# Kernel tuning notes

Measured on AMD Instinct MI355X. Metric: run time of the kernel, lower is better.

The kernel has to match this reference:

```python
import jax, jax.numpy as jnp
import numpy as np

# Config matching init_kwargs
DIM = 768; NH = 12; K = 16; BASE_LR = 1.0  # mini_batch_size K, ttt_base_lr


def _ln(x, g, b, eps=1e-6):
    mu = x.mean(-1, keepdims=True)
    var = x.var(-1, keepdims=True)
    return g * (x - mu) * jax.lax.rsqrt(var + eps) + b


def _ln_l2_bwd(x, tgt, g, b, eps=1e-6):
    # grad wrt x of ||LN(x; g, b) - tgt||^2 (TTT fused layernorm-l2 backward)
    D = x.shape[-1]
    mu = x.mean(-1, keepdims=True)
    var = x.var(-1, keepdims=True)
    std = jnp.sqrt(var + eps)
    xh = (x - mu) / std
    gout = (g * xh + b) - tgt
    gxh = gout * g
    return (D * gxh - gxh.sum(-1, keepdims=True) - xh * (gxh * xh).sum(-1, keepdims=True)) / (D * std)


def _rotary(x, fc):
    # x: [..., N, hd]; fc: [N, hd//2] complex
    xr = x.reshape(*x.shape[:-1], -1, 2)
    xc = jax.lax.complex(xr[..., 0], xr[..., 1]) * fc
    return jnp.stack([jnp.real(xc), jnp.imag(xc)], -1).reshape(x.shape)


def setup_inputs() -> dict:
    key = jax.random.key(0)
    ks = jax.random.split(key, 6)
    B, N, C = 16, 1024, DIM
    nh2, hd, W2 = 2 * NH, C // NH, 2 * C
    f = jnp.float32
    x = jax.random.normal(ks[0], (B, N, C), f)
    qkv_w = jax.random.normal(ks[1], (C, 3 * C), f) * (1.0 / np.sqrt(C))
    proj_w = jax.random.normal(ks[2], (C, C), f) * (1.0 / np.sqrt(C))
    proj_b = jnp.zeros((C,), f)
    W1 = jax.random.normal(ks[3], (nh2, hd, hd), f) * 0.02  # per-head fast-weight init
    b1 = jnp.zeros((nh2, 1, hd), f)
    ttt_ln_w = jnp.ones((nh2, hd), f)
    ttt_ln_b = jnp.zeros((nh2, hd), f)
    post_ln_w = jnp.ones((W2,), f)
    post_ln_b = jnp.zeros((W2,), f)
    lr_w = jax.random.normal(ks[4], (W2, nh2), f) * 0.02  # learnable ttt lr projection
    lr_b = jnp.zeros((nh2,), f)
    token_idx_delta = jnp.zeros((K,), f)  # learnable token-idx offset, init 0
    return dict(x=x, qkv_w=qkv_w, proj_w=proj_w, proj_b=proj_b, W1=W1, b1=b1,
                ttt_ln_w=ttt_ln_w, ttt_ln_b=ttt_ln_b, post_ln_w=post_ln_w, post_ln_b=post_ln_b,
                lr_w=lr_w, lr_b=lr_b, token_idx_delta=token_idx_delta)


def reference(x, qkv_w, proj_w, proj_b, W1, b1, ttt_ln_w, ttt_ln_b,
              post_ln_w, post_ln_b, lr_w, lr_b, token_idx_delta):
    B, N, C = x.shape
    nh2, hd, W2 = 2 * NH, C // NH, 2 * C
    nmb = N // K
    # fused QKV projection (no bias)
    q, k, v = jnp.split(x @ qkv_w, 3, axis=-1)  # each [B,N,C]
    # bidirectional: concat forward stream with token-flipped backward stream
    qq = jnp.concatenate([q, jnp.flip(q, axis=-2)], axis=-1)  # [B,N,2C]
    kk = jnp.concatenate([k, jnp.flip(k, axis=-2)], axis=-1)
    vv = jnp.concatenate([v, jnp.flip(v, axis=-2)], axis=-1)
    xx = jnp.concatenate([x, jnp.flip(x, axis=-2)], axis=-1)

    def heads(t):  # [B,N,2C] -> [B,nh2,N,hd]
        return t.reshape(B, N, nh2, hd).transpose(0, 2, 1, 3)
    XQ, XK, XV = heads(qq), heads(kk), heads(vv)

    # rotary embedding with position_ids % mini_batch_size
    pos = (jnp.arange(N) % K).astype(jnp.float32)
    inv = 1.0 / (10000.0 ** (jnp.arange(0, hd, 2, dtype=jnp.float32) / hd))
    ang = pos[:, None] * inv[None, :]
    fc = jax.lax.complex(jnp.cos(ang), jnp.sin(ang))  # [N, hd//2]
    XQ = _rotary(XQ, fc)
    XK = _rotary(XK, fc)

    def mb(t):  # [B,nh2,N,hd] -> [B,nh2,nmb,K,hd]
        return t.reshape(B, nh2, nmb, K, hd)
    XQ, XK, XV = mb(XQ), mb(XK), mb(XV)

    # eta: token_idx (1/i, learnable offset, clipped) x per-token learnable lr
    Xr = xx.reshape(B, nmb, K, W2)
    lr = jax.nn.sigmoid(Xr @ lr_w + lr_b) * (BASE_LR / hd)  # [B,nmb,K,nh2]
    tok = jnp.clip(1.0 / jnp.arange(1, K + 1, dtype=jnp.float32) + token_idx_delta, 0.0)
    # eta[b,h,m,i,j] = tok[i] * lr[b,m,j,h]
    eta = tok[None, None, None, :, None] * lr.transpose(0, 3, 1, 2)[:, :, :, None, :]  # [B,nh2,nmb,K,K]

    mask = jnp.tril(jnp.ones((K, K), x.dtype))  # AR mask within mini-batch
    g = ttt_ln_w[None, :, None, :]   # [1,nh2,1,hd]
    bt = ttt_ln_b[None, :, None, :]
    W1_0 = jnp.broadcast_to(W1[None], (B, nh2, hd, hd))
    b1_0 = jnp.broadcast_to(b1[None], (B, nh2, 1, hd))

    def step(carry, inp):
        W, bb = carry
        xq, xk, xv, et = inp  # [B,nh2,K,hd] x3, [B,nh2,K,K]
        Z1 = xk @ W + bb
        grad = _ln_l2_bwd(Z1, xv - xk, g, bt)  # dl/dZ1
        attn = jnp.einsum('bhid,bhjd->bhij', xq, xk) * mask
        b1_bar = bb - (et * mask) @ grad
        Z1_bar = xq @ W - (et * attn) @ grad + b1_bar
        last = et[..., -1, :, None]  # eta row of last token [B,nh2,K,1]
        Wn = W - jnp.einsum('bhkd,bhke->bhde', last * xk, grad)
        bn = bb - (last * grad).sum(-2, keepdims=True)
        out = xq + _ln(Z1_bar, g, bt)  # residual + per-head TTT layernorm
        return (Wn, bn), out

    xs = (XQ.transpose(2, 0, 1, 3, 4), XK.transpose(2, 0, 1, 3, 4),
          XV.transpose(2, 0, 1, 3, 4), eta.transpose(2, 0, 1, 3, 4))
    _, Z = jax.lax.scan(step, (W1_0, b1_0), xs)  # Z: [nmb,B,nh2,K,hd]

    Z = Z.transpose(1, 2, 0, 3, 4).reshape(B, nh2, N, hd).transpose(0, 2, 1, 3).reshape(B, N, W2)
    Z = _ln(Z, post_ln_w, post_ln_b)  # mult_norm post-norm
    zf, zb = jnp.split(Z, 2, axis=-1)
    out = zf * jnp.flip(zb, axis=-2)  # merge forward / flipped-backward streams
    return out @ proj_w + proj_b
```

## Files before the change

### kernel.cpp

```cpp
#include <hip/hip_runtime.h>
#include <hip/hip_bf16.h>

#define Bq   16
#define Nseq 1024
#define Cdim 768
#define NH2  24
#define W2D  1536
#define KB   16
#define NMB  64

typedef short bfrag8 __attribute__((ext_vector_type(8)));
typedef short bfrag4 __attribute__((ext_vector_type(4)));
typedef float f32x4  __attribute__((ext_vector_type(4)));

__device__ __forceinline__ short f2bs(float x) {
  union { __hip_bfloat16 b; short s; } u;
  u.b = __float2bfloat16(x);
  return u.s;
}
__device__ __forceinline__ bfrag8 cvt8(const float* v) {
  bfrag8 r;
#pragma unroll
  for (int i = 0; i < 8; ++i) r[i] = f2bs(v[i]);
  return r;
}
__device__ __forceinline__ bfrag4 cvt4(float a, float b, float c, float d) {
  bfrag4 r;
  r[0] = f2bs(a); r[1] = f2bs(b); r[2] = f2bs(c); r[3] = f2bs(d);
  return r;
}
__device__ __forceinline__ void async_copy16(const void* g, void* l) {
  __builtin_amdgcn_global_load_lds((const __attribute__((address_space(1))) void*)g,
                                   (__attribute__((address_space(3))) void*)l, 16, 0, 0);
}

#if defined(__has_builtin)
#  if __has_builtin(__builtin_amdgcn_mfma_f32_16x16x16bf16_1k)
#    define HAVE_MFMA16X16X16 1
#  endif
#endif
__device__ __forceinline__ f32x4 mfma16(bfrag4 a, bfrag4 b, f32x4 c) {
#ifdef HAVE_MFMA16X16X16
  return __builtin_amdgcn_mfma_f32_16x16x16bf16_1k(a, b, c, 0, 0, 0);
#else
  f32x4 d;
  asm volatile("v_mfma_f32_16x16x16_bf16 %0, %1, %2, %3"
               : "=v"(d) : "v"(a), "v"(b), "v"(c));
  return d;
#endif
}

__device__ __forceinline__ void lds_fence() {
  asm volatile("s_waitcnt lgkmcnt(0)" ::: "memory");
  __builtin_amdgcn_sched_barrier(0);
}

template<int N>
__device__ __forceinline__ float dpp_ror(float x) {
  union { float f; int i; } a, r;
  a.f = x;
  r.i = __builtin_amdgcn_update_dpp(0, a.i, 0x120 | N, 0xF, 0xF, 1);
  return r.f;
}
__device__ __forceinline__ float rowsum16(float x) {
  x += dpp_ror<8>(x);
  x += dpp_ror<4>(x);
  x += dpp_ror<2>(x);
  x += dpp_ror<1>(x);
  return x;
}

__global__ __launch_bounds__(256) void gemm_bf16_kernel(
    const __hip_bfloat16* __restrict__ A,
    const __hip_bfloat16* __restrict__ Bt,
    const float* __restrict__ bias, float* __restrict__ C,
    int M, int Kd, int Nd)
{
  __shared__ short sA[128 * 64];
  __shared__ short sB[128 * 64];
  const int t = threadIdx.x;
  const int w = t >> 6, lane = t & 63;
  const int quad = lane >> 4, li = lane & 15;
  const int wm = w & 1, wn = w >> 1;
  const int m0 = blockIdx.y * 128, n0 = blockIdx.x * 128;

  f32x4 acc[4][4];
#pragma unroll
  for (int mt = 0; mt < 4; ++mt)
#pragma unroll
    for (int nt = 0; nt < 4; ++nt) acc[mt][nt] = (f32x4){0.f, 0.f, 0.f, 0.f};

  const __hip_bfloat16* Ab = A + (size_t)m0 * Kd;
  const __hip_bfloat16* Bb = Bt + (size_t)n0 * Kd;

#pragma unroll 1
  for (int k0 = 0; k0 < Kd; k0 += 64) {
    __syncthreads();
#pragma unroll
    for (int i = 0; i < 4; ++i) {
      int c = i * 256 + t;
      int row = c >> 3;
      int gl = (c & 7) ^ (row & 7);
      async_copy16(Ab + (size_t)row * Kd + k0 + gl * 8, &sA[c * 8]);
      async_copy16(Bb + (size_t)row * Kd + k0 + gl * 8, &sB[c * 8]);
    }
    __syncthreads();
#pragma unroll
    for (int ks = 0; ks < 2; ++ks) {
      bfrag8 aF[4], bF[4];
#pragma unroll
      for (int mt = 0; mt < 4; ++mt) {
        int row = wm * 64 + mt * 16 + li;
        int gi = (ks * 4 + quad) ^ (row & 7);
        aF[mt] = *(const bfrag8*)(&sA[row * 64 + gi * 8]);
      }
#pragma unroll
      for (int nt = 0; nt < 4; ++nt) {
        int row = wn * 64 + nt * 16 + li;
        int gi = (ks * 4 + quad) ^ (row & 7);
        bF[nt] = *(const bfrag8*)(&sB[row * 64 + gi * 8]);
      }
#pragma unroll
      for (int mt = 0; mt < 4; ++mt)
#pragma unroll
        for (int nt = 0; nt < 4; ++nt)
          acc[mt][nt] = __builtin_amdgcn_mfma_f32_16x16x32_bf16(aF[mt], bF[nt], acc[mt][nt], 0, 0, 0);
    }
  }

#pragma unroll
  for (int mt = 0; mt < 4; ++mt)
#pragma unroll
    for (int nt = 0; nt < 4; ++nt) {
      int ncol = n0 + wn * 64 + nt * 16 + li;
      float bv = bias ? bias[ncol] : 0.f;
#pragma unroll
      for (int r = 0; r < 4; ++r) {
        int mrow = m0 + wm * 64 + mt * 16 + quad * 4 + r;
        C[(size_t)mrow * Nd + ncol] = acc[mt][nt][r] + bv;
      }
    }
}

__global__ __launch_bounds__(256) void cast_bf16_kernel(
    const float* __restrict__ in, __hip_bfloat16* __restrict__ out, int n4)
{
  int i = blockIdx.x * 256 + threadIdx.x;
  if (i >= n4) return;
  float4 v = ((const float4*)in)[i];
  union { short b[4]; short4 s; } u;
  u.b[0] = f2bs(v.x); u.b[1] = f2bs(v.y); u.b[2] = f2bs(v.z); u.b[3] = f2bs(v.w);
  ((short4*)out)[i] = u.s;
}

__global__ __launch_bounds__(256) void transpose_cast_kernel(
    const float* __restrict__ B, __hip_bfloat16* __restrict__ Bt, int Kd, int Nd)
{
  __shared__ float tl[64][65];
  int k0 = blockIdx.x * 64, n0 = blockIdx.y * 64;
  int tx = threadIdx.x & 63, ty = threadIdx.x >> 6;
#pragma unroll
  for (int i = 0; i < 16; ++i) {
    int k = ty + i * 4;
    tl[k][tx] = B[(size_t)(k0 + k) * Nd + n0 + tx];
  }
  __syncthreads();
#pragma unroll
  for (int i = 0; i < 16; ++i) {
    int n = ty + i * 4;
    Bt[(size_t)(n0 + n) * Kd + k0 + tx] = __float2bfloat16(tl[tx][n]);
  }
}

__global__ __launch_bounds__(64) void lr_kernel(
    const float* __restrict__ x, const float* __restrict__ lr_w,
    const float* __restrict__ lr_b, float* __restrict__ lrout)
{
  const int row = blockIdx.x;
  const int b = row >> 10, n = row & 1023;
  const int l = threadIdx.x;
  const float* x1 = x + (size_t)row * Cdim;
  const float* x2 = x + (size_t)(b * Nseq + (Nseq - 1 - n)) * Cdim;

  float acc[NH2];
#pragma unroll
  for (int hh = 0; hh < NH2; ++hh) acc[hh] = 0.f;

#pragma unroll 1
  for (int i = 0; i < 12; ++i) {
    int c = l + 64 * i;
    float xv1 = x1[c];
    float xv2 = x2[c];
    const float4* w1 = (const float4*)(lr_w + (size_t)c * NH2);
    const float4* w2 = (const float4*)(lr_w + (size_t)(Cdim + c) * NH2);
#pragma unroll
    for (int q4 = 0; q4 < 6; ++q4) {
      float4 wa = w1[q4], wb = w2[q4];
      acc[q4 * 4 + 0] += xv1 * wa.x + xv2 * wb.x;
      acc[q4 * 4 + 1] += xv1 * wa.y + xv2 * wb.y;
      acc[q4 * 4 + 2] += xv1 * wa.z + xv2 * wb.z;
      acc[q4 * 4 + 3] += xv1 * wa.w + xv2 * wb.w;
    }
  }
#pragma unroll
  for (int hh = 0; hh < NH2; ++hh) {
    float s = rowsum16(acc[hh]);
    s += __shfl_xor(s, 16);
    s += __shfl_xor(s, 32);
    acc[hh] = s;
  }
  float mine = 0.f;
#pragma unroll
  for (int hh = 0; hh < NH2; ++hh) mine = (l == hh) ? acc[hh] : mine;
  if (l < NH2) {
    float a = mine + lr_b[l];
    float sg = 1.f / (1.f + expf(-a));
    lrout[(size_t)row * NH2 + l] = sg * (1.f / 64.f);
  }
}

__global__ __launch_bounds__(64, 1) void ttt_scan_kernel(
    const float* __restrict__ qkv,
    const float* __restrict__ lrg,
    const float* __restrict__ W1,
    const float* __restrict__ b1g,
    const float* __restrict__ lnw,
    const float* __restrict__ lnb,
    const float* __restrict__ tid,
    float* __restrict__ Zout)
{
  __shared__ float sQ[16 * 68], sK[16 * 68], sV[16 * 68];

  const int l = threadIdx.x;
  const int quad = l >> 4, li = l & 15;
  const int bh = blockIdx.x, b = bh / NH2, h = bh % NH2;
  const int chan = (h < 12) ? h * 64 : (h - 12) * 64;
  const bool flip = (h >= 12);
  const int bN = b * Nseq;

  float Wf[4][4][4];
  bfrag4 wB[4][4];
#pragma unroll
  for (int t = 0; t < 4; ++t)
#pragma unroll
    for (int kk = 0; kk < 4; ++kk) {
#pragma unroll
      for (int j = 0; j < 4; ++j)
        Wf[t][kk][j] = W1[h * 4096 + (kk * 16 + quad * 4 + j) * 64 + t * 16 + li];
      wB[t][kk] = cvt4(Wf[t][kk][0], Wf[t][kk][1], Wf[t][kk][2], Wf[t][kk][3]);
    }
  float bC[4], gv[4], bt_[4];
#pragma unroll
  for (int t = 0; t < 4; ++t) {
    bC[t]  = b1g[h * 64 + t * 16 + li];
    gv[t]  = lnw[h * 64 + t * 16 + li];
    bt_[t] = lnb[h * 64 + t * 16 + li];
  }

  float tokL;
  {
    float tk = 1.f / (float)(li + 1) + tid[li];
    tokL = tk > 0.f ? tk : 0.f;
  }
  float t15 = 1.f / 16.f + tid[15];
  t15 = t15 > 0.f ? t15 : 0.f;

  float c8[8], s8[8];
  {
    int pos = l >> 2;
#pragma unroll
    for (int pl = 0; pl < 8; ++pl) {
      int p = (l & 3) * 8 + pl;
      float inv = __expf(-((float)(2 * p) * (1.f / 64.f)) * 9.210340371976184f);
      float a = (float)pos * inv;
      c8[pl] = cosf(a);
      s8[pl] = sinf(a);
    }
  }

  float4 pf[3][4];
  float pflr[4];
  {
    int nn = l >> 2;
    int grow = flip ? (bN + Nseq - 1 - nn) : (bN + nn);
#pragma unroll
    for (int a = 0; a < 3; ++a) {
      const float* bse = qkv + (size_t)grow * 2304 + chan + a * 768 + (l & 3) * 16;
#pragma unroll
      for (int i = 0; i < 4; ++i) pf[a][i] = ((const float4*)bse)[i];
    }
#pragma unroll
    for (int r = 0; r < 4; ++r)
      pflr[r] = lrg[(size_t)(bN + quad * 4 + r) * NH2 + h];
  }

#pragma unroll 1
  for (int m = 0; m < NMB; ++m) {
    const int n0 = m * KB;

#pragma unroll
    for (int a = 0; a < 3; ++a) {
      float v16[16];
      *(float4*)(v16)      = pf[a][0]; *(float4*)(v16 + 4)  = pf[a][1];
      *(float4*)(v16 + 8)  = pf[a][2]; *(float4*)(v16 + 12) = pf[a][3];
      if (a < 2) {
#pragma unroll
        for (int pl = 0; pl < 8; ++pl) {
          float e = v16[2 * pl], o = v16[2 * pl + 1];
          v16[2 * pl]     = e * c8[pl] - o * s8[pl];
          v16[2 * pl + 1] = o * c8[pl] + e * s8[pl];
        }
      }
      float* dst = (a == 0 ? sQ : (a == 1 ? sK : sV)) + (l >> 2) * 68 + (l & 3) * 16;
#pragma unroll
      for (int i = 0; i < 4; ++i) ((f32x4*)dst)[i] = *(f32x4*)(v16 + 4 * i);
    }
    float lr4[4];
#pragma unroll
    for (int r = 0; r < 4; ++r) lr4[r] = pflr[r];
    lds_fence();

    if (m < NMB - 1) {
      int nn = (m + 1) * KB + (l >> 2);
      int grow = flip ? (bN + Nseq - 1 - nn) : (bN + nn);
#pragma unroll
      for (int a = 0; a < 3; ++a) {
        const float* bse = qkv + (size_t)grow * 2304 + chan + a * 768 + (l & 3) * 16;
#pragma unroll
        for (int i = 0; i < 4; ++i) pf[a][i] = ((const float4*)bse)[i];
      }
#pragma unroll
      for (int r = 0; r < 4; ++r)
        pflr[r] = lrg[(size_t)(bN + (m + 1) * KB + quad * 4 + r) * NH2 + h];
    }

    bfrag4 aQ4[4], aK4[4];
#pragma unroll
    for (int kk = 0; kk < 4; ++kk) {
      f32x4 q4 = *(const f32x4*)(&sQ[li * 68 + kk * 16 + quad * 4]);
      f32x4 k4 = *(const f32x4*)(&sK[li * 68 + kk * 16 + quad * 4]);
      aQ4[kk] = cvt4(q4[0], q4[1], q4[2], q4[3]);
      aK4[kk] = cvt4(k4[0], k4[1], k4[2], k4[3]);
    }
    float kC[4][4], vC[4][4];
#pragma unroll
    for (int t = 0; t < 4; ++t)
#pragma unroll
      for (int r = 0; r < 4; ++r) {
        int off = (quad * 4 + r) * 68 + t * 16 + li;
        kC[t][r] = sK[off]; vC[t][r] = sV[off];
      }

    f32x4 accZ[4], accQ[4];
#pragma unroll
    for (int t = 0; t < 4; ++t) {
      accZ[t] = (f32x4){0.f, 0.f, 0.f, 0.f};
      accQ[t] = (f32x4){0.f, 0.f, 0.f, 0.f};
#pragma unroll
      for (int kk = 0; kk < 4; ++kk) {
        accZ[t] = mfma16(aK4[kk], wB[t][kk], accZ[t]);
        accQ[t] = mfma16(aQ4[kk], wB[t][kk], accQ[t]);
      }
    }
    f32x4 accAT = (f32x4){0.f, 0.f, 0.f, 0.f};
#pragma unroll
    for (int kk = 0; kk < 4; ++kk)
      accAT = mfma16(aK4[kk], aQ4[kk], accAT);

    bfrag4 aCoef;
    {
      float cf[4];
#pragma unroll
      for (int r = 0; r < 4; ++r) {
        int j = quad * 4 + r;
        cf[r] = (j <= li) ? (-tokL * (accAT[r] + 1.f)) : 0.f;
      }
      aCoef = cvt4(cf[0], cf[1], cf[2], cf[3]);
    }

    float gs[4][4];
#pragma unroll
    for (int r = 0; r < 4; ++r) {
      float zt[4], xht[4], gxht[4];
      float s1 = 0.f, s2 = 0.f;
#pragma unroll
      for (int t = 0; t < 4; ++t) {
        zt[t] = accZ[t][r] + bC[t];
        s1 += zt[t];
        s2 += zt[t] * zt[t];
      }
      s1 = rowsum16(s1);
      s2 = rowsum16(s2);
      float mu = s1 * 0.015625f;
      float var = s2 * 0.015625f - mu * mu;
      float rstd = rsqrtf(var + 1e-6f);
      float r1 = 0.f, r2 = 0.f;
#pragma unroll
      for (int t = 0; t < 4; ++t) {
        xht[t] = (zt[t] - mu) * rstd;
        float gout = gv[t] * xht[t] + bt_[t] - (vC[t][r] - kC[t][r]);
        gxht[t] = gout * gv[t];
        r1 += gxht[t];
        r2 += gxht[t] * xht[t];
      }
      r1 = rowsum16(r1);
      r2 = rowsum16(r2);
      float lrr = lr4[r];
#pragma unroll
      for (int t = 0; t < 4; ++t) {
        float gd = (64.f * gxht[t] - r1 - xht[t] * r2) * rstd * 0.015625f;
        gs[t][r] = lrr * gd;
      }
    }

    bfrag4 bGrad[4], aXk[4];
#pragma unroll
    for (int t = 0; t < 4; ++t) {
      bGrad[t] = cvt4(gs[t][0], gs[t][1], gs[t][2], gs[t][3]);
      aXk[t]   = cvt4(kC[t][0], kC[t][1], kC[t][2], kC[t][3]);
    }

    f32x4 zb[4];
#pragma unroll
    for (int t = 0; t < 4; ++t) {
      f32x4 acc = accQ[t];
#pragma unroll
      for (int r = 0; r < 4; ++r) acc[r] += bC[t];
      zb[t] = mfma16(aCoef, bGrad[t], acc);
    }
#pragma unroll
    for (int r = 0; r < 4; ++r) {
      float s1 = 0.f, s2 = 0.f;
#pragma unroll
      for (int t = 0; t < 4; ++t) { s1 += zb[t][r]; s2 += zb[t][r] * zb[t][r]; }
      s1 = rowsum16(s1);
      s2 = rowsum16(s2);
      float mu = s1 * 0.015625f;
      float var = s2 * 0.015625f - mu * mu;
      float rstd = rsqrtf(var + 1e-6f);
#pragma unroll
      for (int t = 0; t < 4; ++t) {
        float qv = sQ[(quad * 4 + r) * 68 + t * 16 + li];
        float outv = qv + gv[t] * (zb[t][r] - mu) * rstd + bt_[t];
        Zout[(size_t)(bN + n0 + quad * 4 + r) * W2D + h * 64 + t * 16 + li] = outv;
      }
    }

#pragma unroll
    for (int mt = 0; mt < 4; ++mt)
#pragma unroll
      for (int t = 0; t < 4; ++t) {
        f32x4 g = mfma16(aXk[mt], bGrad[t], (f32x4){0.f, 0.f, 0.f, 0.f});
#pragma unroll
        for (int r = 0; r < 4; ++r) Wf[t][mt][r] -= t15 * g[r];
        wB[t][mt] = cvt4(Wf[t][mt][0], Wf[t][mt][1], Wf[t][mt][2], Wf[t][mt][3]);
      }
#pragma unroll
    for (int t = 0; t < 4; ++t) {
      float g0 = gs[t][0] + gs[t][1] + gs[t][2] + gs[t][3];
      g0 += __shfl_xor(g0, 16);
      g0 += __shfl_xor(g0, 32);
      bC[t] -= t15 * g0;
    }
  }
}

__global__ __launch_bounds__(256) void postln_mult_kernel(
    const float* __restrict__ Z, const float* __restrict__ wv,
    const float* __restrict__ bb, __hip_bfloat16* __restrict__ hbuf)
{
  __shared__ float red[16];
  const int pair = blockIdx.x;
  const int b = pair >> 9, n = pair & 511;
  const size_t r1 = (size_t)b * Nseq + n;
  const size_t r2 = (size_t)b * Nseq + (Nseq - 1 - n);
  const float* z1 = Z + r1 * W2D;
  const float* z2 = Z + r2 * W2D;
  const int t = threadIdx.x;

  float v1[6], v2[6];
  float s1a = 0.f, s2a = 0.f, s1b = 0.f, s2b = 0.f;
#pragma unroll
  for (int r = 0; r < 6; ++r) {
    int c = t + 256 * r;
    float a = z1[c]; v1[r] = a; s1a += a; s2a += a * a;
    float d = z2[c]; v2[r] = d; s1b += d; s2b += d * d;
  }
#pragma unroll
  for (int o = 1; o < 64; o <<= 1) {
    s1a += __shfl_xor(s1a, o); s2a += __shfl_xor(s2a, o);
    s1b += __shfl_xor(s1b, o); s2b += __shfl_xor(s2b, o);
  }
  if ((t & 63) == 0) {
    int w = t >> 6;
    red[w] = s1a; red[4 + w] = s2a; red[8 + w] = s1b; red[12 + w] = s2b;
  }
  __syncthreads();
  s1a = red[0] + red[1] + red[2] + red[3];
  s2a = red[4] + red[5] + red[6] + red[7];
  s1b = red[8] + red[9] + red[10] + red[11];
  s2b = red[12] + red[13] + red[14] + red[15];
  float mu1 = s1a * (1.f / 1536.f);
  float var1 = s2a * (1.f / 1536.f) - mu1 * mu1;
  float rstd1 = rsqrtf(var1 + 1e-6f);
  float mu2 = s1b * (1.f / 1536.f);
  float var2 = s2b * (1.f / 1536.f) - mu2 * mu2;
  float rstd2 = rsqrtf(var2 + 1e-6f);
#pragma unroll
  for (int r = 0; r < 3; ++r) {
    int c = t + 256 * r;
    float a1  = wv[c] * (v1[r] - mu1) * rstd1 + bb[c];
    float a1b = wv[c + 768] * (v1[r + 3] - mu1) * rstd1 + bb[c + 768];
    float a2  = wv[c] * (v2[r] - mu2) * rstd2 + bb[c];
    float a2b = wv[c + 768] * (v2[r + 3] - mu2) * rstd2 + bb[c + 768];
    union { __hip_bfloat16 h; short s; } u1, u2;
    u1.h = __float2bfloat16(a1 * a2b);
    u2.h = __float2bfloat16(a2 * a1b);
    ((short*)hbuf)[r1 * Cdim + c] = u1.s;
    ((short*)hbuf)[r2 * Cdim + c] = u2.s;
  }
}

extern "C" void kernel_launch(void* const* d_in, const int* in_sizes, int n_in,
                              void* d_out, int out_size, void* d_ws, size_t ws_size,
                              hipStream_t stream)
{
  const float* x         = (const float*)d_in[0];
  const float* qkv_w     = (const float*)d_in[1];
  const float* proj_w    = (const float*)d_in[2];
  const float* proj_b    = (const float*)d_in[3];
  const float* W1        = (const float*)d_in[4];
  const float* b1        = (const float*)d_in[5];
  const float* ttt_ln_w  = (const float*)d_in[6];
  const float* ttt_ln_b  = (const float*)d_in[7];
  const float* post_ln_w = (const float*)d_in[8];
  const float* post_ln_b = (const float*)d_in[9];
  const float* lr_w      = (const float*)d_in[10];
  const float* lr_b      = (const float*)d_in[11];
  const float* tid       = (const float*)d_in[12];
  float* out = (float*)d_out;
  float* ws  = (float*)d_ws;

  float* qkv   = ws;
  float* lrbuf = ws + 37748736;
  float* Zbuf  = ws + 38141952;
  __hip_bfloat16* xbf    = (__hip_bfloat16*)(ws + 38141952);
  __hip_bfloat16* wqkv_t = (__hip_bfloat16*)(ws + 44433408);
  __hip_bfloat16* hbf    = (__hip_bfloat16*)(ws + 25165824);
  __hip_bfloat16* wproj_t= (__hip_bfloat16*)(ws + 37748736);

  const int Mrows = Bq * Nseq;

  cast_bf16_kernel<<<(Mrows * Cdim / 4 + 255) / 256, 256, 0, stream>>>(x, xbf, Mrows * Cdim / 4);
  {
    dim3 g(Cdim / 64, 3 * Cdim / 64);
    transpose_cast_kernel<<<g, 256, 0, stream>>>(qkv_w, wqkv_t, Cdim, 3 * Cdim);
  }
  {
    dim3 g(3 * Cdim / 128, Mrows / 128);
    gemm_bf16_kernel<<<g, 256, 0, stream>>>(xbf, wqkv_t, nullptr, qkv, Mrows, Cdim, 3 * Cdim);
  }
  lr_kernel<<<Mrows, 64, 0, stream>>>(x, lr_w, lr_b, lrbuf);

  ttt_scan_kernel<<<Bq * NH2, 64, 0, stream>>>(qkv, lrbuf, W1, b1, ttt_ln_w, ttt_ln_b, tid, Zbuf);

  postln_mult_kernel<<<Bq * Nseq / 2, 256, 0, stream>>>(Zbuf, post_ln_w, post_ln_b, hbf);
  {
    dim3 g(Cdim / 64, Cdim / 64);
    transpose_cast_kernel<<<g, 256, 0, stream>>>(proj_w, wproj_t, Cdim, Cdim);
  }
  {
    dim3 g(Cdim / 128, Mrows / 128);
    gemm_bf16_kernel<<<g, 256, 0, stream>>>(hbf, wproj_t, proj_b, out, Mrows, Cdim, Cdim);
  }
}
```

Before: 616.7 us.

## Double-buffer TTT scan LDS staging with transposed copies and remap GEMM blocks per XCD

The TTT scan kernel now double-buffers its Q/K/V LDS tiles and prefetches two mini-batches ahead, so the next chunk is staged while the current one is computed. It also stores transposed copies of Q, K and V so the per-column operand reads become vectorized f32x4 loads instead of scalar strided reads. The bias update is moved earlier. Separately, the GEMM launch becomes a 1D grid whose block index is remapped round-robin across the 8 XCDs for better L2 locality. The cost is more LDS, extra transposed LDS writes, and higher register pressure in a single-wave kernel.

```diff
diff --git a/kernel.cpp b/kernel.cpp
--- a/kernel.cpp
+++ b/kernel.cpp
@@ -74,7 +74,7 @@
     const __hip_bfloat16* __restrict__ A,
     const __hip_bfloat16* __restrict__ Bt,
     const float* __restrict__ bias, float* __restrict__ C,
-    int M, int Kd, int Nd)
+    int M, int Kd, int Nd, int gx)
 {
   __shared__ short sA[128 * 64];
   __shared__ short sB[128 * 64];
@@ -82,7 +82,11 @@
   const int w = t >> 6, lane = t & 63;
   const int quad = lane >> 4, li = lane & 15;
   const int wm = w & 1, wn = w >> 1;
-  const int m0 = blockIdx.y * 128, n0 = blockIdx.x * 128;
+
+  const int nwg = gridDim.x;
+  const int q8 = nwg >> 3;
+  const int lid = ((int)blockIdx.x & 7) * q8 + ((int)blockIdx.x >> 3);
+  const int m0 = (lid / gx) * 128, n0 = (lid % gx) * 128;
 
   f32x4 acc[4][4];
 #pragma unroll
@@ -229,7 +233,11 @@
     const float* __restrict__ tid,
     float* __restrict__ Zout)
 {
-  __shared__ float sQ[16 * 68], sK[16 * 68], sV[16 * 68];
+  __shared__ float sQb[2][16 * 68];
+  __shared__ float sKb[2][16 * 68];
+  __shared__ float sQT[2][64 * 20];
+  __shared__ float sKT[2][64 * 20];
+  __shared__ float sVT[2][64 * 20];
 
   const int l = threadIdx.x;
   const int quad = l >> 4, li = l & 15;
@@ -237,6 +245,7 @@
   const int chan = (h < 12) ? h * 64 : (h - 12) * 64;
   const bool flip = (h >= 12);
   const int bN = b * Nseq;
+  const int stok = l >> 2, sc0 = (l & 3) * 16;
 
   float Wf[4][4][4];
   bfrag4 wB[4][4];
@@ -267,37 +276,30 @@
 
   float c8[8], s8[8];
   {
-    int pos = l >> 2;
 #pragma unroll
     for (int pl = 0; pl < 8; ++pl) {
       int p = (l & 3) * 8 + pl;
       float inv = __expf(-((float)(2 * p) * (1.f / 64.f)) * 9.210340371976184f);
-      float a = (float)pos * inv;
+      float a = (float)stok * inv;
       c8[pl] = cosf(a);
       s8[pl] = sinf(a);
     }
   }
 
   float4 pf[3][4];
-  float pflr[4];
-  {
-    int nn = l >> 2;
+  float lrcur[4], pfl[4];
+
+  auto issue_qkv = [&](int mt) {
+    int nn = mt * KB + stok;
     int grow = flip ? (bN + Nseq - 1 - nn) : (bN + nn);
 #pragma unroll
     for (int a = 0; a < 3; ++a) {
-      const float* bse = qkv + (size_t)grow * 2304 + chan + a * 768 + (l & 3) * 16;
+      const float* bse = qkv + (size_t)grow * 2304 + chan + a * 768 + sc0;
 #pragma unroll
       for (int i = 0; i < 4; ++i) pf[a][i] = ((const float4*)bse)[i];
     }
-#pragma unroll
-    for (int r = 0; r < 4; ++r)
-      pflr[r] = lrg[(size_t)(bN + quad * 4 + r) * NH2 + h];
-  }
-
-#pragma unroll 1
-  for (int m = 0; m < NMB; ++m) {
-    const int n0 = m * KB;
-
+  };
+  auto stage = [&](int buf) {
 #pragma unroll
     for (int a = 0; a < 3; ++a) {
       float v16[16];
@@ -311,45 +313,73 @@
           v16[2 * pl + 1] = o * c8[pl] + e * s8[pl];
         }
       }
-      float* dst = (a == 0 ? sQ : (a == 1 ? sK : sV)) + (l >> 2) * 68 + (l & 3) * 16;
-#pragma unroll
-      for (int i = 0; i < 4; ++i) ((f32x4*)dst)[i] = *(f32x4*)(v16 + 4 * i);
+      if (a == 0) {
+        float* dst = &sQb[buf][stok * 68 + sc0];
+#pragma unroll
+        for (int i = 0; i < 4; ++i) ((f32x4*)dst)[i] = *(f32x4*)(v16 + 4 * i);
+#pragma unroll
+        for (int i = 0; i < 16; ++i) sQT[buf][(sc0 + i) * 20 + stok] = v16[i];
+      } else if (a == 1) {
+        float* dst = &sKb[buf][stok * 68 + sc0];
+#pragma unroll
+        for (int i = 0; i < 4; ++i) ((f32x4*)dst)[i] = *(f32x4*)(v16 + 4 * i);
+#pragma unroll
+        for (int i = 0; i < 16; ++i) sKT[buf][(sc0 + i) * 20 + stok] = v16[i];
+      } else {
+#pragma unroll
+        for (int i = 0; i < 16; ++i) sVT[buf][(sc0 + i) * 20 + stok] = v16[i];
+      }
+    }
+  };
+
+  issue_qkv(0);
+#pragma unroll
+  for (int r = 0; r < 4; ++r) lrcur[r] = lrg[(size_t)(bN + quad * 4 + r) * NH2 + h];
+  stage(0);
+  issue_qkv(1);
+#pragma unroll
+  for (int r = 0; r < 4; ++r) pfl[r] = lrg[(size_t)(bN + KB + quad * 4 + r) * NH2 + h];
+  lds_fence();
+
+#pragma unroll 1
+  for (int m = 0; m < NMB; ++m) {
+    const int n0 = m * KB;
+    const int cur = m & 1, alt = cur ^ 1;
+
+    f32x4 q4[4], k4[4];
+#pragma unroll
+    for (int kk = 0; kk < 4; ++kk) {
+      k4[kk] = *(const f32x4*)(&sKb[cur][li * 68 + kk * 16 + quad * 4]);
+      q4[kk] = *(const f32x4*)(&sQb[cur][li * 68 + kk * 16 + quad * 4]);
+    }
+    f32x4 kC[4], vC[4];
+#pragma unroll
+    for (int t = 0; t < 4; ++t) {
+      kC[t] = *(const f32x4*)(&sKT[cur][(t * 16 + li) * 20 + quad * 4]);
+      vC[t] = *(const f32x4*)(&sVT[cur][(t * 16 + li) * 20 + quad * 4]);
     }
     float lr4[4];
 #pragma unroll
-    for (int r = 0; r < 4; ++r) lr4[r] = pflr[r];
-    lds_fence();
+    for (int r = 0; r < 4; ++r) lr4[r] = lrcur[r];
 
     if (m < NMB - 1) {
-      int nn = (m + 1) * KB + (l >> 2);
-      int grow = flip ? (bN + Nseq - 1 - nn) : (bN + nn);
-#pragma unroll
-      for (int a = 0; a < 3; ++a) {
-        const float* bse = qkv + (size_t)grow * 2304 + chan + a * 768 + (l & 3) * 16;
-#pragma unroll
-        for (int i = 0; i < 4; ++i) pf[a][i] = ((const float4*)bse)[i];
-      }
-#pragma unroll
-      for (int r = 0; r < 4; ++r)
-        pflr[r] = lrg[(size_t)(bN + (m + 1) * KB + quad * 4 + r) * NH2 + h];
+      stage(alt);
+#pragma unroll
+      for (int r = 0; r < 4; ++r) lrcur[r] = pfl[r];
+      if (m < NMB - 2) {
+        issue_qkv(m + 2);
+#pragma unroll
+        for (int r = 0; r < 4; ++r)
+          pfl[r] = lrg[(size_t)(bN + (m + 2) * KB + quad * 4 + r) * NH2 + h];
+      }
     }
 
     bfrag4 aQ4[4], aK4[4];
 #pragma unroll
     for (int kk = 0; kk < 4; ++kk) {
-      f32x4 q4 = *(const f32x4*)(&sQ[li * 68 + kk * 16 + quad * 4]);
-      f32x4 k4 = *(const f32x4*)(&sK[li * 68 + kk * 16 + quad * 4]);
-      aQ4[kk] = cvt4(q4[0], q4[1], q4[2], q4[3]);
-      aK4[kk] = cvt4(k4[0], k4[1], k4[2], k4[3]);
-    }
-    float kC[4][4], vC[4][4];
-#pragma unroll
-    for (int t = 0; t < 4; ++t)
-#pragma unroll
-      for (int r = 0; r < 4; ++r) {
-        int off = (quad * 4 + r) * 68 + t * 16 + li;
-        kC[t][r] = sK[off]; vC[t][r] = sV[off];
-      }
+      aK4[kk] = cvt4(k4[kk][0], k4[kk][1], k4[kk][2], k4[kk][3]);
+      aQ4[kk] = cvt4(q4[kk][0], q4[kk][1], q4[kk][2], q4[kk][3]);
+    }
 
     f32x4 accZ[4], accQ[4];
 #pragma unroll
@@ -428,6 +458,19 @@
       for (int r = 0; r < 4; ++r) acc[r] += bC[t];
       zb[t] = mfma16(aCoef, bGrad[t], acc);
     }
+
+#pragma unroll
+    for (int t = 0; t < 4; ++t) {
+      float g0 = gs[t][0] + gs[t][1] + gs[t][2] + gs[t][3];
+      g0 += __shfl_xor(g0, 16);
+      g0 += __shfl_xor(g0, 32);
+      bC[t] -= t15 * g0;
+    }
+
+    f32x4 qC[4];
+#pragma unroll
+    for (int t = 0; t < 4; ++t)
+      qC[t] = *(const f32x4*)(&sQT[cur][(t * 16 + li) * 20 + quad * 4]);
 #pragma unroll
     for (int r = 0; r < 4; ++r) {
       float s1 = 0.f, s2 = 0.f;
@@ -440,8 +483,7 @@
       float rstd = rsqrtf(var + 1e-6f);
 #pragma unroll
       for (int t = 0; t < 4; ++t) {
-        float qv = sQ[(quad * 4 + r) * 68 + t * 16 + li];
-        float outv = qv + gv[t] * (zb[t][r] - mu) * rstd + bt_[t];
+        float outv = qC[t][r] + gv[t] * (zb[t][r] - mu) * rstd + bt_[t];
         Zout[(size_t)(bN + n0 + quad * 4 + r) * W2D + h * 64 + t * 16 + li] = outv;
       }
     }
@@ -455,13 +497,8 @@
         for (int r = 0; r < 4; ++r) Wf[t][mt][r] -= t15 * g[r];
         wB[t][mt] = cvt4(Wf[t][mt][0], Wf[t][mt][1], Wf[t][mt][2], Wf[t][mt][3]);
       }
-#pragma unroll
-    for (int t = 0; t < 4; ++t) {
-      float g0 = gs[t][0] + gs[t][1] + gs[t][2] + gs[t][3];
-      g0 += __shfl_xor(g0, 16);
-      g0 += __shfl_xor(g0, 32);
-      bC[t] -= t15 * g0;
-    }
+
+    lds_fence();
   }
 }
 
@@ -557,8 +594,9 @@
     transpose_cast_kernel<<<g, 256, 0, stream>>>(qkv_w, wqkv_t, Cdim, 3 * Cdim);
   }
   {
-    dim3 g(3 * Cdim / 128, Mrows / 128);
-    gemm_bf16_kernel<<<g, 256, 0, stream>>>(xbf, wqkv_t, nullptr, qkv, Mrows, Cdim, 3 * Cdim);
+    int gx = 3 * Cdim / 128;
+    int nwg = gx * (Mrows / 128);
+    gemm_bf16_kernel<<<nwg, 256, 0, stream>>>(xbf, wqkv_t, nullptr, qkv, Mrows, Cdim, 3 * Cdim, gx);
   }
   lr_kernel<<<Mrows, 64, 0, stream>>>(x, lr_w, lr_b, lrbuf);
 
@@ -570,7 +608,8 @@
     transpose_cast_kernel<<<g, 256, 0, stream>>>(proj_w, wproj_t, Cdim, Cdim);
   }
   {
-    dim3 g(Cdim / 128, Mrows / 128);
-    gemm_bf16_kernel<<<g, 256, 0, stream>>>(hbf, wproj_t, proj_b, out, Mrows, Cdim, Cdim);
-  }
-}
+    int gx = Cdim / 128;
+    int nwg = gx * (Mrows / 128);
+    gemm_bf16_kernel<<<nwg, 256, 0, stream>>>(hbf, wproj_t, proj_b, out, Mrows, Cdim, Cdim, gx);
+  }
+}
```

Result: slower. 653.2 us (+5.9%).

## Fuse bf16 cast into lr kernel, stage GEMM epilogue via LDS, remap workgroups

Applied to the files above, without the earlier changes.

Removes the separate cast_bf16 kernel and writes the bf16 copy of x from the lr-projection kernel, which now handles a forward/reversed row pair per block so each x row is read once. The GEMM epilogue stages each accumulator tile through per-wave LDS and stores it with 16-byte vector writes instead of scattered scalar stores. The GEMM also uses a 1D grid with a block-index remap across groups of 8, meant to improve L2 locality across XCDs. The trade-offs are extra LDS per block, which may lower occupancy, and scalar short writes of the bf16 x.

```diff
diff --git a/kernel.cpp b/kernel.cpp
--- a/kernel.cpp
+++ b/kernel.cpp
@@ -74,15 +74,20 @@
     const __hip_bfloat16* __restrict__ A,
     const __hip_bfloat16* __restrict__ Bt,
     const float* __restrict__ bias, float* __restrict__ C,
-    int M, int Kd, int Nd)
+    int M, int Kd, int Nd, int gx)
 {
   __shared__ short sA[128 * 64];
   __shared__ short sB[128 * 64];
+  __shared__ float sEp[4][16 * 68];
   const int t = threadIdx.x;
   const int w = t >> 6, lane = t & 63;
   const int quad = lane >> 4, li = lane & 15;
   const int wm = w & 1, wn = w >> 1;
-  const int m0 = blockIdx.y * 128, n0 = blockIdx.x * 128;
+
+  const int nwg = gridDim.x;
+  const int q8 = nwg >> 3;
+  const int lid = ((int)blockIdx.x & 7) * q8 + ((int)blockIdx.x >> 3);
+  const int m0 = (lid / gx) * 128, n0 = (lid % gx) * 128;
 
   f32x4 acc[4][4];
 #pragma unroll
@@ -128,29 +133,29 @@
     }
   }
 
-#pragma unroll
-  for (int mt = 0; mt < 4; ++mt)
+  float* ep = sEp[w];
+  const int erow = lane >> 2, ecb = lane & 3;
+#pragma unroll
+  for (int mt = 0; mt < 4; ++mt) {
 #pragma unroll
     for (int nt = 0; nt < 4; ++nt) {
       int ncol = n0 + wn * 64 + nt * 16 + li;
       float bv = bias ? bias[ncol] : 0.f;
 #pragma unroll
-      for (int r = 0; r < 4; ++r) {
-        int mrow = m0 + wm * 64 + mt * 16 + quad * 4 + r;
-        C[(size_t)mrow * Nd + ncol] = acc[mt][nt][r] + bv;
-      }
-    }
-}
-
-__global__ __launch_bounds__(256) void cast_bf16_kernel(
-    const float* __restrict__ in, __hip_bfloat16* __restrict__ out, int n4)
-{
-  int i = blockIdx.x * 256 + threadIdx.x;
-  if (i >= n4) return;
-  float4 v = ((const float4*)in)[i];
-  union { short b[4]; short4 s; } u;
-  u.b[0] = f2bs(v.x); u.b[1] = f2bs(v.y); u.b[2] = f2bs(v.z); u.b[3] = f2bs(v.w);
-  ((short4*)out)[i] = u.s;
+      for (int r = 0; r < 4; ++r)
+        ep[(quad * 4 + r) * 68 + nt * 16 + li] = acc[mt][nt][r] + bv;
+    }
+    lds_fence();
+    {
+      size_t rbase = (size_t)(m0 + wm * 64 + mt * 16 + erow) * Nd + n0 + wn * 64 + ecb * 16;
+#pragma unroll
+      for (int j = 0; j < 4; ++j) {
+        f32x4 v = *(const f32x4*)(&ep[erow * 68 + ecb * 16 + 4 * j]);
+        *(f32x4*)(&C[rbase + 4 * j]) = v;
+      }
+    }
+    lds_fence();
+  }
 }
 
 __global__ __launch_bounds__(256) void transpose_cast_kernel(
@@ -172,50 +177,67 @@
   }
 }
 
-__global__ __launch_bounds__(64) void lr_kernel(
+__global__ __launch_bounds__(64) void lrcast_kernel(
     const float* __restrict__ x, const float* __restrict__ lr_w,
-    const float* __restrict__ lr_b, float* __restrict__ lrout)
+    const float* __restrict__ lr_b, float* __restrict__ lrout,
+    __hip_bfloat16* __restrict__ xbf)
 {
-  const int row = blockIdx.x;
-  const int b = row >> 10, n = row & 1023;
+  const int pair = blockIdx.x;
+  const int b = pair >> 9, n = pair & 511;
+  const size_t r1 = (size_t)b * Nseq + n;
+  const size_t r2 = (size_t)b * Nseq + (Nseq - 1 - n);
   const int l = threadIdx.x;
-  const float* x1 = x + (size_t)row * Cdim;
-  const float* x2 = x + (size_t)(b * Nseq + (Nseq - 1 - n)) * Cdim;
-
-  float acc[NH2];
-#pragma unroll
-  for (int hh = 0; hh < NH2; ++hh) acc[hh] = 0.f;
+  const float* x1 = x + r1 * Cdim;
+  const float* x2 = x + r2 * Cdim;
+
+  float a1[NH2], a2[NH2];
+#pragma unroll
+  for (int hh = 0; hh < NH2; ++hh) { a1[hh] = 0.f; a2[hh] = 0.f; }
 
 #pragma unroll 1
   for (int i = 0; i < 12; ++i) {
     int c = l + 64 * i;
     float xv1 = x1[c];
     float xv2 = x2[c];
-    const float4* w1 = (const float4*)(lr_w + (size_t)c * NH2);
-    const float4* w2 = (const float4*)(lr_w + (size_t)(Cdim + c) * NH2);
+    ((short*)xbf)[r1 * Cdim + c] = f2bs(xv1);
+    ((short*)xbf)[r2 * Cdim + c] = f2bs(xv2);
+    const float4* wlo = (const float4*)(lr_w + (size_t)c * NH2);
+    const float4* whi = (const float4*)(lr_w + (size_t)(Cdim + c) * NH2);
 #pragma unroll
     for (int q4 = 0; q4 < 6; ++q4) {
-      float4 wa = w1[q4], wb = w2[q4];
-      acc[q4 * 4 + 0] += xv1 * wa.x + xv2 * wb.x;
-      acc[q4 * 4 + 1] += xv1 * wa.y + xv2 * wb.y;
-      acc[q4 * 4 + 2] += xv1 * wa.z + xv2 * wb.z;
-      acc[q4 * 4 + 3] += xv1 * wa.w + xv2 * wb.w;
+      float4 wa = wlo[q4], wb = whi[q4];
+      a1[q4 * 4 + 0] += xv1 * wa.x + xv2 * wb.x;
+      a1[q4 * 4 + 1] += xv1 * wa.y + xv2 * wb.y;
+      a1[q4 * 4 + 2] += xv1 * wa.z + xv2 * wb.z;
+      a1[q4 * 4 + 3] += xv1 * wa.w + xv2 * wb.w;
+      a2[q4 * 4 + 0] += xv2 * wa.x + xv1 * wb.x;
+      a2[q4 * 4 + 1] += xv2 * wa.y + xv1 * wb.y;
+      a2[q4 * 4 + 2] += xv2 * wa.z + xv1 * wb.z;
+      a2[q4 * 4 + 3] += xv2 * wa.w + xv1 * wb.w;
     }
   }
 #pragma unroll
   for (int hh = 0; hh < NH2; ++hh) {
-    float s = rowsum16(acc[hh]);
+    float s = rowsum16(a1[hh]);
     s += __shfl_xor(s, 16);
     s += __shfl_xor(s, 32);
-    acc[hh] = s;
-  }
-  float mine = 0.f;
-#pragma unroll
-  for (int hh = 0; hh < NH2; ++hh) mine = (l == hh) ? acc[hh] : mine;
+    a1[hh] = s;
+    float u = rowsum16(a2[hh]);
+    u += __shfl_xor(u, 16);
+    u += __shfl_xor(u, 32);
+    a2[hh] = u;
+  }
+  float m1 = 0.f, m2 = 0.f;
+#pragma unroll
+  for (int hh = 0; hh < NH2; ++hh) {
+    m1 = (l == hh) ? a1[hh] : m1;
+    m2 = (l == hh) ? a2[hh] : m2;
+  }
   if (l < NH2) {
-    float a = mine + lr_b[l];
-    float sg = 1.f / (1.f + expf(-a));
-    lrout[(size_t)row * NH2 + l] = sg * (1.f / 64.f);
+    float v1 = m1 + lr_b[l];
+    float v2 = m2 + lr_b[l];
+    lrout[r1 * NH2 + l] = (1.f / (1.f + expf(-v1))) * (1.f / 64.f);
+    lrout[r2 * NH2 + l] = (1.f / (1.f + expf(-v2))) * (1.f / 64.f);
   }
 }
 
@@ -551,16 +573,16 @@
 
   const int Mrows = Bq * Nseq;
 
-  cast_bf16_kernel<<<(Mrows * Cdim / 4 + 255) / 256, 256, 0, stream>>>(x, xbf, Mrows * Cdim / 4);
   {
     dim3 g(Cdim / 64, 3 * Cdim / 64);
     transpose_cast_kernel<<<g, 256, 0, stream>>>(qkv_w, wqkv_t, Cdim, 3 * Cdim);
   }
-  {
-    dim3 g(3 * Cdim / 128, Mrows / 128);
-    gemm_bf16_kernel<<<g, 256, 0, stream>>>(xbf, wqkv_t, nullptr, qkv, Mrows, Cdim, 3 * Cdim);
-  }
-  lr_kernel<<<Mrows, 64, 0, stream>>>(x, lr_w, lr_b, lrbuf);
+  lrcast_kernel<<<Mrows / 2, 64, 0, stream>>>(x, lr_w, lr_b, lrbuf, xbf);
+  {
+    int gx = 3 * Cdim / 128;
+    int nwg = gx * (Mrows / 128);
+    gemm_bf16_kernel<<<nwg, 256, 0, stream>>>(xbf, wqkv_t, nullptr, qkv, Mrows, Cdim, 3 * Cdim, gx);
+  }
 
   ttt_scan_kernel<<<Bq * NH2, 64, 0, stream>>>(qkv, lrbuf, W1, b1, ttt_ln_w, ttt_ln_b, tid, Zbuf);
 
@@ -570,7 +592,8 @@
     transpose_cast_kernel<<<g, 256, 0, stream>>>(proj_w, wproj_t, Cdim, Cdim);
   }
   {
-    dim3 g(Cdim / 128, Mrows / 128);
-    gemm_bf16_kernel<<<g, 256, 0, stream>>>(hbf, wproj_t, proj_b, out, Mrows, Cdim, Cdim);
-  }
-}
+    int gx = Cdim / 128;
+    int nwg = gx * (Mrows / 128);
+    gemm_bf16_kernel<<<nwg, 256, 0, stream>>>(hbf, wproj_t, proj_b, out, Mrows, Cdim, Cdim, gx);
+  }
+}
```

After: 520.7 us. -15.6%, faster.
